# Optimization experiments

Measured on AMD Instinct MI355X. Metric: run time of the kernel, lower is better.

## Reference

```python
import jax, jax.numpy as jnp
import numpy as np

N_NODES = 10000
N_EDGES = 160000
F_IN = 50          # PPI num_features
H = 4              # attention heads
C_BODY = 256       # body GAT out channels per head -> concat 1024
C_HEAD = 64        # head GAT out channels per head -> concat 256
T = 121            # PPI num_classes (one task head each)
D_BODY = H * C_BODY   # 1024
D_HEAD = H * C_HEAD   # 256


def setup_inputs() -> dict:
    key = jax.random.key(0)
    ks = jax.random.split(key, 18)
    inv = lambda f: 1.0 / np.sqrt(f)
    x = jax.random.normal(ks[0], (N_NODES, F_IN), dtype=jnp.float32)
    edge_index = jax.random.randint(ks[1], (2, N_EDGES), 0, N_NODES, dtype=jnp.int64)
    # body GATConv(50 -> 256, heads=4)
    W_body = jax.random.normal(ks[2], (F_IN, H, C_BODY), jnp.float32) * inv(F_IN)
    a_src_body = jax.random.normal(ks[3], (H, C_BODY), jnp.float32) * 0.1
    a_dst_body = jax.random.normal(ks[4], (H, C_BODY), jnp.float32) * 0.1
    b_body = jnp.zeros((D_BODY,), jnp.float32)
    # body Linear(50 -> 1024)
    Wfc_body = jax.random.normal(ks[5], (F_IN, D_BODY), jnp.float32) * inv(F_IN)
    bfc_body = jnp.zeros((D_BODY,), jnp.float32)
    # stacked per-task head GATConv(1024 -> 64, heads=4)
    Wh = jax.random.normal(ks[6], (T, D_BODY, H, C_HEAD), jnp.float32) * inv(D_BODY)
    a_src_h = jax.random.normal(ks[7], (T, H, C_HEAD), jnp.float32) * 0.1
    a_dst_h = jax.random.normal(ks[8], (T, H, C_HEAD), jnp.float32) * 0.1
    b_h = jnp.zeros((T, D_HEAD), jnp.float32)
    # stacked per-task Linear(1024 -> 256)
    W1 = jax.random.normal(ks[9], (T, D_BODY, D_HEAD), jnp.float32) * inv(D_BODY)
    b1 = jnp.zeros((T, D_HEAD), jnp.float32)
    # stacked per-task Linear(256 -> 2)
    W2 = jax.random.normal(ks[10], (T, D_HEAD, 2), jnp.float32) * inv(D_HEAD)
    b2 = jnp.zeros((T, 2), jnp.float32)
    return dict(x=x, edge_index=edge_index,
                W_body=W_body, a_src_body=a_src_body, a_dst_body=a_dst_body, b_body=b_body,
                Wfc_body=Wfc_body, bfc_body=bfc_body,
                Wh=Wh, a_src_h=a_src_h, a_dst_h=a_dst_h, b_h=b_h,
                W1=W1, b1=b1, W2=W2, b2=b2)


def gat_conv(x, W, a_src, a_dst, bias, src, dst, num_nodes):
    """PyG GATConv (concat=True, negative_slope=0.2). src/dst include self loops."""
    h = jnp.einsum('nf,fhc->nhc', x, W)                      # [N,H,C]
    al_src = jnp.sum(h * a_src, axis=-1)                     # [N,H]
    al_dst = jnp.sum(h * a_dst, axis=-1)                     # [N,H]
    e = jax.nn.leaky_relu(al_src[src] + al_dst[dst], 0.2)    # [E,H]
    # segment softmax over incoming edges of each target node
    m = jax.lax.stop_gradient(jax.ops.segment_max(e, dst, num_segments=num_nodes))
    ex = jnp.exp(e - m[dst])
    denom = jax.ops.segment_sum(ex, dst, num_segments=num_nodes)
    alpha = ex / (denom[dst] + 1e-16)                        # [E,H]
    out = jax.ops.segment_sum(alpha[:, :, None] * h[src], dst, num_segments=num_nodes)
    return out.reshape(num_nodes, -1) + bias                 # [N,H*C]


def reference(x, edge_index, W_body, a_src_body, a_dst_body, b_body,
              Wfc_body, bfc_body, Wh, a_src_h, a_dst_h, b_h, W1, b1, W2, b2):
    n = x.shape[0]
    loops = jnp.arange(n, dtype=edge_index.dtype)
    src = jnp.concatenate([edge_index[0], loops])   # add_self_loops=True
    dst = jnp.concatenate([edge_index[1], loops])
    x1 = jax.nn.elu(gat_conv(x, W_body, a_src_body, a_dst_body, b_body, src, dst, n)
                    + x @ Wfc_body + bfc_body)      # [N,1024]

    def head(params):
        Wh_t, as_t, ad_t, bh_t, W1_t, b1_t, W2_t, b2_t = params
        xh = jax.nn.elu(gat_conv(x1, Wh_t, as_t, ad_t, bh_t, src, dst, n)
                        + x1 @ W1_t + b1_t)         # [N,256]
        return xh @ W2_t + b2_t                     # [N,2]

    out = jax.lax.map(head, (Wh, a_src_h, a_dst_h, b_h, W1, b1, W2, b2))
    return out  # [T, N, 2], stacked version of the original list of 121 outputs
```

## Files before the change

kernel.cpp:

```cpp
#include <hip/hip_runtime.h>

typedef unsigned short u16;
typedef unsigned int u32;
typedef __attribute__((ext_vector_type(8))) short short8;
typedef __attribute__((ext_vector_type(4))) float f32x4;

#define NN 10000
#define NE 160000
#define ET 170000
#define FI 50
#define DB 1024
#define NT 121

static __device__ __forceinline__ float bf2f(u16 b) { return __uint_as_float(((u32)b) << 16); }
static __device__ __forceinline__ u16 f2bf(float f) {
  u32 u = __float_as_uint(f);
  u += 0x7FFFu + ((u >> 16) & 1u);
  return (u16)(u >> 16);
}
static __device__ __forceinline__ float eluf(float x) { return x > 0.f ? x : __expf(x) - 1.f; }
static __device__ __forceinline__ float lrelu(float x) { return x > 0.f ? x : 0.2f * x; }

__device__ __forceinline__ void gload16(const void* g, void* l) {
  __builtin_amdgcn_global_load_lds((const __attribute__((address_space(1))) u32*)g,
                                   (__attribute__((address_space(3))) u32*)l, 16, 0, 0);
}

__global__ __launch_bounds__(256) void k_detect(const int* __restrict__ ei, int* flag) {
  int any = 0;
  for (int i = threadIdx.x; i < NE; i += 256) any |= ei[2 * i + 1];
  if (any) flag[0] = 1;
}

__global__ __launch_bounds__(256) void k_deg(const int* __restrict__ ei, const int* __restrict__ flag,
                                             int* deg) {
  int e = blockIdx.x * 256 + threadIdx.x;
  if (e >= ET) return;
  int is32 = flag[0];
  int d = (e < NE) ? (is32 ? ei[NE + e] : ei[2 * (NE + e)]) : (e - NE);
  atomicAdd(&deg[d], 1);
}

__global__ __launch_bounds__(256) void k_scan(const int* __restrict__ deg, int* __restrict__ rowptr) {
  __shared__ int ps[256];
  int tid = threadIdx.x;
  int s = 0;
  for (int i = 0; i < 40; i++) { int idx = tid * 40 + i; if (idx < NN) s += deg[idx]; }
  ps[tid] = s;
  __syncthreads();
  if (tid == 0) {
    int run = 0;
    for (int i = 0; i < 256; i++) { int v = ps[i]; ps[i] = run; run += v; }
    rowptr[NN] = run;
  }
  __syncthreads();
  int run = ps[tid];
  for (int i = 0; i < 40; i++) {
    int idx = tid * 40 + i;
    if (idx < NN) { rowptr[idx] = run; run += deg[idx]; }
  }
}

__global__ __launch_bounds__(256) void k_fill(const int* __restrict__ ei, const int* __restrict__ flag,
                                              const int* __restrict__ rowptr, int* fill, int* csr) {
  int e = blockIdx.x * 256 + threadIdx.x;
  if (e >= ET) return;
  int is32 = flag[0];
  int s, d;
  if (e < NE) { s = is32 ? ei[e] : ei[2 * e]; d = is32 ? ei[NE + e] : ei[2 * (NE + e)]; }
  else { s = d = e - NE; }
  int pos = atomicAdd(&fill[d], 1);
  csr[rowptr[d] + pos] = s;
}

__global__ __launch_bounds__(256) void k_body_gemm(const float* __restrict__ x, const float* __restrict__ Wb,
                                                   const float* __restrict__ Wfc,
                                                   u16* __restrict__ h_body, u16* __restrict__ xfc) {
  __shared__ float xs[32][52];
  int tid = threadIdx.x;
  int m0 = blockIdx.x * 32;
  for (int i = tid; i < 32 * FI; i += 256) {
    int r = i / FI, c = i - r * FI;
    int row = m0 + r; if (row > NN - 1) row = NN - 1;
    xs[r][c] = x[(size_t)row * FI + c];
  }
  __syncthreads();
  int col = blockIdx.y * 256 + tid;
  const float* Wp; u16* op;
  if (col < DB) { Wp = Wb + col; op = h_body + col; }
  else { Wp = Wfc + (col - DB); op = xfc + (col - DB); }
  float acc[32];
  #pragma unroll
  for (int m = 0; m < 32; m++) acc[m] = 0.f;
  for (int k = 0; k < FI; k++) {
    float wv = Wp[(size_t)k * DB];
    #pragma unroll
    for (int m = 0; m < 32; m++) acc[m] += xs[m][k] * wv;
  }
  #pragma unroll
  for (int m = 0; m < 32; m++) {
    int row = m0 + m;
    if (row < NN) op[(size_t)row * DB] = f2bf(acc[m]);
  }
}

__global__ __launch_bounds__(64) void k_body_al(const u16* __restrict__ h_body, const float* __restrict__ as,
                                                const float* __restrict__ ad, float* __restrict__ al) {
  int n = blockIdx.x, l = threadIdx.x;
  const u16* hr = h_body + (size_t)n * DB + l * 16;
  const float* ap = as + l * 16;
  const float* dp = ad + l * 16;
  float ss = 0.f, sd = 0.f;
  #pragma unroll
  for (int i = 0; i < 16; i++) { float hv = bf2f(hr[i]); ss += hv * ap[i]; sd += hv * dp[i]; }
  #pragma unroll
  for (int o = 1; o < 16; o <<= 1) { ss += __shfl_xor(ss, o); sd += __shfl_xor(sd, o); }
  if ((l & 15) == 0) { int h = l >> 4; al[(size_t)n * 8 + h] = ss; al[(size_t)n * 8 + 4 + h] = sd; }
}

__global__ __launch_bounds__(256) void k_body_agg(const u16* __restrict__ h_body, const u16* __restrict__ xfc,
                                                  const float* __restrict__ al, const int* __restrict__ rowptr,
                                                  const int* __restrict__ csr, const float* __restrict__ bb,
                                                  const float* __restrict__ bfc, u16* __restrict__ x1b) {
  __shared__ float wl[256];
  __shared__ int sl[64];
  int n = blockIdx.x, tid = threadIdx.x;
  int c0 = tid * 4, h = tid >> 6;
  float acc0 = 0, acc1 = 0, acc2 = 0, acc3 = 0, wsum = 0;
  int beg = rowptr[n], end = rowptr[n + 1];
  for (int base = beg; base < end; base += 64) {
    int cnt = end - base; if (cnt > 64) cnt = 64;
    int slot = tid >> 2, hh = tid & 3;
    if (slot < cnt) {
      int s = csr[base + slot];
      if (hh == 0) sl[slot] = s;
      float e = al[(size_t)s * 8 + hh] + al[(size_t)n * 8 + 4 + hh];
      wl[slot * 4 + hh] = __expf(lrelu(e));
    }
    __syncthreads();
    for (int j = 0; j < cnt; j++) {
      float wv = wl[j * 4 + h];
      int s = sl[j];
      ushort4 hv = *(const ushort4*)(h_body + (size_t)s * DB + c0);
      acc0 += wv * bf2f(hv.x); acc1 += wv * bf2f(hv.y);
      acc2 += wv * bf2f(hv.z); acc3 += wv * bf2f(hv.w);
      wsum += wv;
    }
    __syncthreads();
  }
  float inv = 1.f / (wsum + 1e-16f);
  ushort4 xf = *(const ushort4*)(xfc + (size_t)n * DB + c0);
  ushort4 o;
  o.x = f2bf(eluf(acc0 * inv + bb[c0 + 0] + bf2f(xf.x) + bfc[c0 + 0]));
  o.y = f2bf(eluf(acc1 * inv + bb[c0 + 1] + bf2f(xf.y) + bfc[c0 + 1]));
  o.z = f2bf(eluf(acc2 * inv + bb[c0 + 2] + bf2f(xf.z) + bfc[c0 + 2]));
  o.w = f2bf(eluf(acc3 * inv + bb[c0 + 3] + bf2f(xf.w) + bfc[c0 + 3]));
  *(ushort4*)(x1b + (size_t)n * DB + c0) = o;
}

__global__ __launch_bounds__(256) void k_trans_w(const float* __restrict__ Wh, const float* __restrict__ W1,
                                                 u16* __restrict__ Wt, int t0) {
  __shared__ float tile[64][65];
  int t = t0 + blockIdx.z;
  int k0 = blockIdx.x * 64, n0 = blockIdx.y * 64;
  const float* Wsrc = (n0 < 256) ? (Wh + (size_t)t * 1024 * 256 + n0)
                                 : (W1 + (size_t)t * 1024 * 256 + (n0 - 256));
  int tid = threadIdx.x;
  for (int i = tid; i < 4096; i += 256) {
    int kr = i >> 6, nc = i & 63;
    tile[kr][nc] = Wsrc[(size_t)(k0 + kr) * 256 + nc];
  }
  __syncthreads();
  u16* dst = Wt + ((size_t)blockIdx.z * 512 + n0) * 1024 + k0;
  for (int i = tid; i < 4096; i += 256) {
    int nr = i >> 6, kc = i & 63;
    dst[(size_t)nr * 1024 + kc] = f2bf(tile[kc][nr]);
  }
}

__global__ __launch_bounds__(256) void k_task_gemm(const u16* __restrict__ x1b, const u16* __restrict__ Wt,
                                                   u16* __restrict__ HT) {
  __shared__ alignas(16) u16 As[4096];
  __shared__ alignas(16) u16 Bs[4096];
  int tid = threadIdx.x;
  int sRow = tid >> 2, sQ = tid & 3;
  int m0 = blockIdx.x * 128;
  int r0 = m0 + sRow; if (r0 > NN - 1) r0 = NN - 1;
  int r1 = m0 + 64 + sRow; if (r1 > NN - 1) r1 = NN - 1;
  const u16* Ag0 = x1b + (size_t)r0 * 1024 + sQ * 8;
  const u16* Ag1 = x1b + (size_t)r1 * 1024 + sQ * 8;
  const u16* Bg0 = Wt + ((size_t)blockIdx.z * 512 + blockIdx.y * 128 + sRow) * 1024 + sQ * 8;
  const u16* Bg1 = Bg0 + (size_t)64 * 1024;
  u16* Al0 = As + tid * 8;
  u16* Al1 = As + 2048 + tid * 8;
  u16* Bl0 = Bs + tid * 8;
  u16* Bl1 = Bs + 2048 + tid * 8;
  int wv = tid >> 6, lane = tid & 63;
  int wm = wv >> 1, wn = wv & 1;
  const u16* Ar = As + ((wm * 64) + (lane & 15)) * 32 + (lane >> 4) * 8;
  const u16* Br = Bs + ((wn * 64) + (lane & 15)) * 32 + (lane >> 4) * 8;
  f32x4 acc[4][4];
  #pragma unroll
  for (int i = 0; i < 4; i++)
    #pragma unroll
    for (int j = 0; j < 4; j++) acc[i][j] = (f32x4){0.f, 0.f, 0.f, 0.f};
  for (int k0 = 0; k0 < 1024; k0 += 32) {
    gload16(Ag0 + k0, Al0);
    gload16(Ag1 + k0, Al1);
    gload16(Bg0 + k0, Bl0);
    gload16(Bg1 + k0, Bl1);
    __syncthreads();
    short8 af[4], bfr[4];
    #pragma unroll
    for (int i = 0; i < 4; i++) af[i] = *(const short8*)(Ar + i * 512);
    #pragma unroll
    for (int i = 0; i < 4; i++) bfr[i] = *(const short8*)(Br + i * 512);
    #pragma unroll
    for (int i = 0; i < 4; i++)
      #pragma unroll
      for (int j = 0; j < 4; j++)
        acc[i][j] = __builtin_amdgcn_mfma_f32_16x16x32_bf16(af[i], bfr[j], acc[i][j], 0, 0, 0);
    __syncthreads();
  }
  u16* Hb = HT + (size_t)blockIdx.z * NN * 512;
  #pragma unroll
  for (int i = 0; i < 4; i++) {
    int rbase = m0 + wm * 64 + i * 16 + (lane >> 4) * 4;
    #pragma unroll
    for (int j = 0; j < 4; j++) {
      int col = blockIdx.y * 128 + wn * 64 + j * 16 + (lane & 15);
      #pragma unroll
      for (int r = 0; r < 4; r++) {
        int row = rbase + r;
        if (row < NN) Hb[(size_t)row * 512 + col] = f2bf(acc[i][j][r]);
      }
    }
  }
}

__global__ __launch_bounds__(64) void k_task_al(const u16* __restrict__ HT, const float* __restrict__ ash,
                                                const float* __restrict__ adh, float* __restrict__ ALt, int t0) {
  int n = blockIdx.x, g = blockIdx.y, l = threadIdx.x;
  int t = t0 + g;
  const u16* row = HT + ((size_t)g * NN + n) * 512 + l * 4;
  ushort4 v = *(const ushort4*)row;
  int h = l >> 4, cl = (l * 4) & 63;
  const float* ap = ash + ((size_t)t * 4 + h) * 64 + cl;
  const float* dp = adh + ((size_t)t * 4 + h) * 64 + cl;
  float f0 = bf2f(v.x), f1 = bf2f(v.y), f2 = bf2f(v.z), f3 = bf2f(v.w);
  float ss = f0 * ap[0] + f1 * ap[1] + f2 * ap[2] + f3 * ap[3];
  float sd = f0 * dp[0] + f1 * dp[1] + f2 * dp[2] + f3 * dp[3];
  #pragma unroll
  for (int o = 1; o < 16; o <<= 1) { ss += __shfl_xor(ss, o); sd += __shfl_xor(sd, o); }
  if ((l & 15) == 0) {
    float* dst = ALt + ((size_t)g * NN + n) * 8;
    dst[h] = ss; dst[4 + h] = sd;
  }
}

__global__ __launch_bounds__(64) void k_task_agg_out(const u16* __restrict__ HT, const float* __restrict__ ALt,
                                                     const int* __restrict__ rowptr, const int* __restrict__ csr,
                                                     const float* __restrict__ bh, const float* __restrict__ b1,
                                                     const float* __restrict__ W2, const float* __restrict__ b2,
                                                     float* __restrict__ out, int t0) {
  __shared__ float wl[256];
  __shared__ int sl[64];
  int n = blockIdx.x, g = blockIdx.y, l = threadIdx.x;
  int t = t0 + g;
  int c0 = l * 4, h = l >> 4;
  const u16* Hb = HT + (size_t)g * NN * 512;
  const float* ALg = ALt + (size_t)g * NN * 8;
  float ad0 = ALg[(size_t)n * 8 + 4], ad1 = ALg[(size_t)n * 8 + 5];
  float ad2 = ALg[(size_t)n * 8 + 6], ad3 = ALg[(size_t)n * 8 + 7];
  float acc0 = 0, acc1 = 0, acc2 = 0, acc3 = 0, wsum = 0;
  int beg = rowptr[n], end = rowptr[n + 1];
  for (int base = beg; base < end; base += 64) {
    int cnt = end - base; if (cnt > 64) cnt = 64;
    if (l < cnt) {
      int s = csr[base + l];
      sl[l] = s;
      const float* alsp = ALg + (size_t)s * 8;
      wl[l * 4 + 0] = __expf(lrelu(alsp[0] + ad0));
      wl[l * 4 + 1] = __expf(lrelu(alsp[1] + ad1));
      wl[l * 4 + 2] = __expf(lrelu(alsp[2] + ad2));
      wl[l * 4 + 3] = __expf(lrelu(alsp[3] + ad3));
    }
    __syncthreads();
    for (int j = 0; j < cnt; j++) {
      float wv = wl[j * 4 + h];
      int s = sl[j];
      ushort4 hv = *(const ushort4*)(Hb + (size_t)s * 512 + c0);
      acc0 += wv * bf2f(hv.x); acc1 += wv * bf2f(hv.y);
      acc2 += wv * bf2f(hv.z); acc3 += wv * bf2f(hv.w);
      wsum += wv;
    }
    __syncthreads();
  }
  float inv = 1.f / (wsum + 1e-16f);
  ushort4 fc = *(const ushort4*)(Hb + (size_t)n * 512 + 256 + c0);
  const float* bhp = bh + (size_t)t * 256 + c0;
  const float* b1p = b1 + (size_t)t * 256 + c0;
  const float* w2p = W2 + ((size_t)t * 256 + c0) * 2;
  float o0 = 0, o1 = 0, xv;
  xv = eluf(acc0 * inv + bhp[0] + bf2f(fc.x) + b1p[0]); o0 += xv * w2p[0]; o1 += xv * w2p[1];
  xv = eluf(acc1 * inv + bhp[1] + bf2f(fc.y) + b1p[1]); o0 += xv * w2p[2]; o1 += xv * w2p[3];
  xv = eluf(acc2 * inv + bhp[2] + bf2f(fc.z) + b1p[2]); o0 += xv * w2p[4]; o1 += xv * w2p[5];
  xv = eluf(acc3 * inv + bhp[3] + bf2f(fc.w) + b1p[3]); o0 += xv * w2p[6]; o1 += xv * w2p[7];
  #pragma unroll
  for (int o = 1; o < 64; o <<= 1) { o0 += __shfl_xor(o0, o); o1 += __shfl_xor(o1, o); }
  if (l == 0) {
    float* op = out + ((size_t)t * NN + n) * 2;
    op[0] = o0 + b2[t * 2];
    op[1] = o1 + b2[t * 2 + 1];
  }
}

extern "C" void kernel_launch(void* const* d_in, const int* in_sizes, int n_in,
                              void* d_out, int out_size, void* d_ws, size_t ws_size,
                              hipStream_t stream) {
  const float* x   = (const float*)d_in[0];
  const int*   ei  = (const int*)  d_in[1];
  const float* Wb  = (const float*)d_in[2];
  const float* asb = (const float*)d_in[3];
  const float* adb = (const float*)d_in[4];
  const float* bb  = (const float*)d_in[5];
  const float* Wfc = (const float*)d_in[6];
  const float* bfc = (const float*)d_in[7];
  const float* Wh  = (const float*)d_in[8];
  const float* ash = (const float*)d_in[9];
  const float* adh = (const float*)d_in[10];
  const float* bh  = (const float*)d_in[11];
  const float* W1  = (const float*)d_in[12];
  const float* b1  = (const float*)d_in[13];
  const float* W2  = (const float*)d_in[14];
  const float* b2  = (const float*)d_in[15];
  float* out = (float*)d_out;

  char* w = (char*)d_ws;
  size_t off = 0;
  auto take = [&](size_t b) { size_t o = off; off = (off + b + 255) & ~(size_t)255; return o; };
  u16*   x1b    = (u16*)  (w + take((size_t)NN * DB * 2));
  float* albody = (float*)(w + take((size_t)NN * 8 * 4));
  int*   flag   = (int*)  (w + take(4 + NN * 4 + NN * 4));
  int*   deg    = flag + 1;
  int*   fill   = deg + NN;
  int*   rowptr = (int*)  (w + take((NN + 1) * 4));
  int*   csr    = (int*)  (w + take((size_t)ET * 4));
  size_t Rbase = off;
  u16* h_body = (u16*)(w + Rbase);
  u16* xfc    = h_body + (size_t)NN * DB;
  const size_t perTask = 1048576 + 10240000 + 320000;
  size_t avail = ws_size > Rbase ? ws_size - Rbase : 0;
  int G = (int)(avail / perTask);
  if (G < 1) G = 1;
  if (G > NT) G = NT;
  u16*   Wt  = (u16*)(w + Rbase);
  u16*   HT  = Wt + (size_t)G * 524288;
  float* ALt = (float*)(HT + (size_t)G * 5120000);

  hipMemsetAsync(flag, 0, 4 + NN * 4 + NN * 4, stream);
  k_detect<<<1, 256, 0, stream>>>(ei, flag);
  k_deg<<<(ET + 255) / 256, 256, 0, stream>>>(ei, flag, deg);
  k_scan<<<1, 256, 0, stream>>>(deg, rowptr);
  k_fill<<<(ET + 255) / 256, 256, 0, stream>>>(ei, flag, rowptr, fill, csr);
  k_body_gemm<<<dim3(313, 8), 256, 0, stream>>>(x, Wb, Wfc, h_body, xfc);
  k_body_al<<<NN, 64, 0, stream>>>(h_body, asb, adb, albody);
  k_body_agg<<<NN, 256, 0, stream>>>(h_body, xfc, albody, rowptr, csr, bb, bfc, x1b);

  for (int t0 = 0; t0 < NT; t0 += G) {
    int Gc = NT - t0; if (Gc > G) Gc = G;
    k_trans_w<<<dim3(16, 8, Gc), 256, 0, stream>>>(Wh, W1, Wt, t0);
    k_task_gemm<<<dim3(79, 4, Gc), 256, 0, stream>>>(x1b, Wt, HT);
    k_task_al<<<dim3(NN, Gc), 64, 0, stream>>>(HT, ash, adh, ALt, t0);
    k_task_agg_out<<<dim3(NN, Gc), 64, 0, stream>>>(HT, ALt, rowptr, csr, bh, b1, W2, b2, out, t0);
  }
}
```

Baseline: 3.613 ms.

## Loop task GEMM over tasks per block with XCD-aware tile mapping

The task GEMM grid drops its per-task z dimension; each of the 316 blocks now loops serially over all Gc tasks in the chunk. Block indices are remapped so each of the 8 XCDs gets a contiguous range of output tiles, which should keep the same x1b row tiles in that XCD's L2 across tasks. Output stores become nontemporal to avoid polluting cache with HT. The cost is far fewer concurrent blocks, so occupancy and latency hiding drop sharply, and there is no double buffering to compensate.

Result: slower. 4.872 ms (+34.9%).

```diff
diff --git a/kernel.cpp b/kernel.cpp
--- a/kernel.cpp
+++ b/kernel.cpp
@@ -179,18 +179,22 @@
 }
 
 __global__ __launch_bounds__(256) void k_task_gemm(const u16* __restrict__ x1b, const u16* __restrict__ Wt,
-                                                   u16* __restrict__ HT) {
+                                                   u16* __restrict__ HT, int Gc) {
   __shared__ alignas(16) u16 As[4096];
   __shared__ alignas(16) u16 Bs[4096];
+  int i = blockIdx.x + 79 * blockIdx.y;
+  int g = i & 7, j = i >> 3;
+  int S = (g < 4) ? g * 40 : 160 + (g - 4) * 39;
+  int L = S + j;
+  int bm = L >> 2, bn = L & 3;
   int tid = threadIdx.x;
   int sRow = tid >> 2, sQ = tid & 3;
-  int m0 = blockIdx.x * 128;
+  int m0 = bm * 128;
   int r0 = m0 + sRow; if (r0 > NN - 1) r0 = NN - 1;
   int r1 = m0 + 64 + sRow; if (r1 > NN - 1) r1 = NN - 1;
   const u16* Ag0 = x1b + (size_t)r0 * 1024 + sQ * 8;
   const u16* Ag1 = x1b + (size_t)r1 * 1024 + sQ * 8;
-  const u16* Bg0 = Wt + ((size_t)blockIdx.z * 512 + blockIdx.y * 128 + sRow) * 1024 + sQ * 8;
-  const u16* Bg1 = Bg0 + (size_t)64 * 1024;
+  const u16* BgBase = Wt + ((size_t)(bn * 128) + sRow) * 1024 + sQ * 8;
   u16* Al0 = As + tid * 8;
   u16* Al1 = As + 2048 + tid * 8;
   u16* Bl0 = Bs + tid * 8;
@@ -199,40 +203,45 @@
   int wm = wv >> 1, wn = wv & 1;
   const u16* Ar = As + ((wm * 64) + (lane & 15)) * 32 + (lane >> 4) * 8;
   const u16* Br = Bs + ((wn * 64) + (lane & 15)) * 32 + (lane >> 4) * 8;
-  f32x4 acc[4][4];
-  #pragma unroll
-  for (int i = 0; i < 4; i++)
+
+  for (int z = 0; z < Gc; z++) {
+    const u16* Bg0 = BgBase + (size_t)z * 524288;
+    const u16* Bg1 = Bg0 + 65536;
+    f32x4 acc[4][4];
     #pragma unroll
-    for (int j = 0; j < 4; j++) acc[i][j] = (f32x4){0.f, 0.f, 0.f, 0.f};
-  for (int k0 = 0; k0 < 1024; k0 += 32) {
-    gload16(Ag0 + k0, Al0);
-    gload16(Ag1 + k0, Al1);
-    gload16(Bg0 + k0, Bl0);
-    gload16(Bg1 + k0, Bl1);
-    __syncthreads();
-    short8 af[4], bfr[4];
+    for (int a = 0; a < 4; a++)
+      #pragma unroll
+      for (int b = 0; b < 4; b++) acc[a][b] = (f32x4){0.f, 0.f, 0.f, 0.f};
+    for (int k0 = 0; k0 < 1024; k0 += 32) {
+      gload16(Ag0 + k0, Al0);
+      gload16(Ag1 + k0, Al1);
+      gload16(Bg0 + k0, Bl0);
+      gload16(Bg1 + k0, Bl1);
+      __syncthreads();
+      short8 af[4], bfr[4];
+      #pragma unroll
+      for (int a = 0; a < 4; a++) af[a] = *(const short8*)(Ar + a * 512);
+      #pragma unroll
+      for (int a = 0; a < 4; a++) bfr[a] = *(const short8*)(Br + a * 512);
+      #pragma unroll
+      for (int a = 0; a < 4; a++)
+        #pragma unroll
+        for (int b = 0; b < 4; b++)
+          acc[a][b] = __builtin_amdgcn_mfma_f32_16x16x32_bf16(af[a], bfr[b], acc[a][b], 0, 0, 0);
+      __syncthreads();
+    }
+    u16* Hb = HT + (size_t)z * NN * 512;
     #pragma unroll
-    for (int i = 0; i < 4; i++) af[i] = *(const short8*)(Ar + i * 512);
-    #pragma unroll
-    for (int i = 0; i < 4; i++) bfr[i] = *(const short8*)(Br + i * 512);
-    #pragma unroll
-    for (int i = 0; i < 4; i++)
-      #pragma unroll
-      for (int j = 0; j < 4; j++)
-        acc[i][j] = __builtin_amdgcn_mfma_f32_16x16x32_bf16(af[i], bfr[j], acc[i][j], 0, 0, 0);
-    __syncthreads();
-  }
-  u16* Hb = HT + (size_t)blockIdx.z * NN * 512;
-  #pragma unroll
-  for (int i = 0; i < 4; i++) {
-    int rbase = m0 + wm * 64 + i * 16 + (lane >> 4) * 4;
-    #pragma unroll
-    for (int j = 0; j < 4; j++) {
-      int col = blockIdx.y * 128 + wn * 64 + j * 16 + (lane & 15);
-      #pragma unroll
-      for (int r = 0; r < 4; r++) {
-        int row = rbase + r;
-        if (row < NN) Hb[(size_t)row * 512 + col] = f2bf(acc[i][j][r]);
+    for (int a = 0; a < 4; a++) {
+      int rbase = m0 + wm * 64 + a * 16 + (lane >> 4) * 4;
+      #pragma unroll
+      for (int b = 0; b < 4; b++) {
+        int col = bn * 128 + wn * 64 + b * 16 + (lane & 15);
+        #pragma unroll
+        for (int r = 0; r < 4; r++) {
+          int row = rbase + r;
+          if (row < NN) __builtin_nontemporal_store(f2bf(acc[a][b][r]), &Hb[(size_t)row * 512 + col]);
+        }
       }
     }
   }
@@ -370,7 +379,7 @@
   for (int t0 = 0; t0 < NT; t0 += G) {
     int Gc = NT - t0; if (Gc > G) Gc = G;
     k_trans_w<<<dim3(16, 8, Gc), 256, 0, stream>>>(Wh, W1, Wt, t0);
-    k_task_gemm<<<dim3(79, 4, Gc), 256, 0, stream>>>(x1b, Wt, HT);
+    k_task_gemm<<<dim3(79, 4), 256, 0, stream>>>(x1b, Wt, HT, Gc);
     k_task_al<<<dim3(NN, Gc), 64, 0, stream>>>(HT, ash, adh, ALt, t0);
     k_task_agg_out<<<dim3(NN, Gc), 64, 0, stream>>>(HT, ALt, rowptr, csr, bh, b1, W2, b2, out, t0);
   }
```
